# Kernel optimization log

Measured on AMD Instinct MI355X. Metric: run time of the kernel, lower is better.

The kernel has to match this reference:

```python
import jax, jax.numpy as jnp
import numpy as np

N_NODES = 20000
N_EDGES = 200000
N_TOK = 8          # N patch tokens per node
IN_DIM = 64        # C
N_HEADS = 4
HEAD_DIM = 16      # out_dim


def setup_inputs() -> dict:
    key = jax.random.key(0)
    ks = jax.random.split(key, 16)
    scale = 1.0 / np.sqrt(IN_DIM).astype(np.float32)
    def lin(i):
        W = jax.random.normal(ks[i], (IN_DIM, N_HEADS * HEAD_DIM), dtype=jnp.float32) * scale
        b = jax.random.normal(ks[i + 1], (N_HEADS * HEAD_DIM,), dtype=jnp.float32) * 0.01
        return W, b
    Qw, Qb = lin(0)
    Kw, Kb = lin(2)
    Vw, Vb = lin(4)
    Ew, Eb = lin(6)
    h = jax.random.normal(ks[8], (N_NODES, N_TOK, IN_DIM), dtype=jnp.float32)
    e = jax.random.normal(ks[9], (N_EDGES, N_TOK, IN_DIM), dtype=jnp.float32)
    src = jax.random.randint(ks[10], (N_EDGES,), 0, N_NODES)
    dst = jax.random.randint(ks[11], (N_EDGES,), 0, N_NODES)
    return {"h": h, "e": e, "src": src, "dst": dst,
            "Qw": Qw, "Qb": Qb, "Kw": Kw, "Kb": Kb,
            "Vw": Vw, "Vb": Vb, "Ew": Ew, "Eb": Eb}


def _proj(x, W, b):
    # x: [M, N, C] -> [M, N, H, D]
    y = x @ W + b
    return y.reshape(x.shape[0], x.shape[1], N_HEADS, HEAD_DIM)


def reference(h, e, src, dst, Qw, Qb, Kw, Kb, Vw, Vb, Ew, Eb):
    Qh = _proj(h, Qw, Qb)   # [n, N, H, D]
    Kh = _proj(h, Kw, Kb)
    Vh = _proj(h, Vw, Vb)
    pe = _proj(e, Ew, Eb)   # [E, N, H, D]
    inv_sqrt_d = jnp.float32(1.0 / np.sqrt(HEAD_DIM))
    # edge-wise elementwise QK score, scaled, plus relative PE
    score = Kh[src] * Qh[dst] * inv_sqrt_d + pe   # [E, N, H, D]
    e_out = score
    # exp of head-dim-summed clamped score
    s = jnp.exp(jnp.clip(jnp.sum(score, axis=-1, keepdims=True), -5.0, 5.0))  # [E, N, H, 1]
    wV = jax.ops.segment_sum(Vh[src] * s, dst, num_segments=N_NODES)  # [n, N, H, D]
    z = jax.ops.segment_sum(s, dst, num_segments=N_NODES)             # [n, N, H, 1]
    h_out = wV / (z + 1e-6)
    return h_out, e_out
```

## Files before the change

### kernel.cpp

```cpp
#include <hip/hip_runtime.h>
#include <hip/hip_bf16.h>

#define IN_DIM 64
#define N_TOK 8
#define OUT_DIM 64
#define HEAD_DIM 16
#define N_HEADS 4

__global__ void zero_kernel(int* p, int n) {
    int i = blockIdx.x * blockDim.x + threadIdx.x;
    if (i < n) p[i] = 0;
}

__global__ void hist_kernel(const int* __restrict__ dst, int* __restrict__ deg, int n) {
    int i = blockIdx.x * blockDim.x + threadIdx.x;
    if (i < n) atomicAdd(&deg[dst[i]], 1);
}

__global__ void scan_kernel(const int* __restrict__ deg, int* __restrict__ offs,
                            int* __restrict__ cur, int n) {
    __shared__ int buf[1024];
    __shared__ int carry;
    const int tid = threadIdx.x;
    if (tid == 0) carry = 0;
    __syncthreads();
    for (int base = 0; base < n; base += 1024) {
        int i = base + tid;
        int v = (i < n) ? deg[i] : 0;
        buf[tid] = v;
        __syncthreads();
        for (int off = 1; off < 1024; off <<= 1) {
            int t = (tid >= off) ? buf[tid - off] : 0;
            __syncthreads();
            buf[tid] += t;
            __syncthreads();
        }
        int incl = buf[tid];
        int excl = incl - v + carry;
        if (i < n) { offs[i] = excl; cur[i] = excl; }
        __syncthreads();
        if (tid == 0) carry += buf[1023];
        __syncthreads();
    }
    if (tid == 0) offs[n] = carry;
}

__global__ void scatter_kernel(const int* __restrict__ dst, int* __restrict__ cur,
                               int* __restrict__ csr, int n) {
    int i = blockIdx.x * blockDim.x + threadIdx.x;
    if (i < n) {
        int pos = atomicAdd(&cur[dst[i]], 1);
        csr[pos] = i;
    }
}

__device__ __forceinline__ void proj16_acc(const float* __restrict__ tile, int lane,
                                           const float* __restrict__ wb,
                                           float acc[16]) {
#pragma unroll 8
    for (int k = 0; k < 64; ++k) {
        const float ev = tile[lane * 65 + k];
        const float4 w0 = *reinterpret_cast<const float4*>(wb + k * 64);
        const float4 w1 = *reinterpret_cast<const float4*>(wb + k * 64 + 4);
        const float4 w2 = *reinterpret_cast<const float4*>(wb + k * 64 + 8);
        const float4 w3 = *reinterpret_cast<const float4*>(wb + k * 64 + 12);
        acc[0]  = fmaf(ev, w0.x, acc[0]);
        acc[1]  = fmaf(ev, w0.y, acc[1]);
        acc[2]  = fmaf(ev, w0.z, acc[2]);
        acc[3]  = fmaf(ev, w0.w, acc[3]);
        acc[4]  = fmaf(ev, w1.x, acc[4]);
        acc[5]  = fmaf(ev, w1.y, acc[5]);
        acc[6]  = fmaf(ev, w1.z, acc[6]);
        acc[7]  = fmaf(ev, w1.w, acc[7]);
        acc[8]  = fmaf(ev, w2.x, acc[8]);
        acc[9]  = fmaf(ev, w2.y, acc[9]);
        acc[10] = fmaf(ev, w2.z, acc[10]);
        acc[11] = fmaf(ev, w2.w, acc[11]);
        acc[12] = fmaf(ev, w3.x, acc[12]);
        acc[13] = fmaf(ev, w3.y, acc[13]);
        acc[14] = fmaf(ev, w3.z, acc[14]);
        acc[15] = fmaf(ev, w3.w, acc[15]);
    }
}

__device__ __forceinline__ void init16_bias(const float* __restrict__ bb, float acc[16]) {
    const float4 b0 = *reinterpret_cast<const float4*>(bb);
    const float4 b1 = *reinterpret_cast<const float4*>(bb + 4);
    const float4 b2 = *reinterpret_cast<const float4*>(bb + 8);
    const float4 b3 = *reinterpret_cast<const float4*>(bb + 12);
    acc[0] = b0.x;  acc[1] = b0.y;  acc[2] = b0.z;  acc[3] = b0.w;
    acc[4] = b1.x;  acc[5] = b1.y;  acc[6] = b1.z;  acc[7] = b1.w;
    acc[8] = b2.x;  acc[9] = b2.y;  acc[10] = b2.z; acc[11] = b2.w;
    acc[12] = b3.x; acc[13] = b3.y; acc[14] = b3.z; acc[15] = b3.w;
}

__device__ __forceinline__ void store16(float* __restrict__ out, const float acc[16],
                                        float scale) {
    *reinterpret_cast<float4*>(out)      = make_float4(acc[0] * scale, acc[1] * scale,
                                                       acc[2] * scale, acc[3] * scale);
    *reinterpret_cast<float4*>(out + 4)  = make_float4(acc[4] * scale, acc[5] * scale,
                                                       acc[6] * scale, acc[7] * scale);
    *reinterpret_cast<float4*>(out + 8)  = make_float4(acc[8] * scale, acc[9] * scale,
                                                       acc[10] * scale, acc[11] * scale);
    *reinterpret_cast<float4*>(out + 12) = make_float4(acc[12] * scale, acc[13] * scale,
                                                       acc[14] * scale, acc[15] * scale);
}

__global__ void __launch_bounds__(256) hproj_kernel(
    const float* __restrict__ h,
    const float* __restrict__ Qw, const float* __restrict__ Qb,
    const float* __restrict__ Kw, const float* __restrict__ Kb,
    const float* __restrict__ Vw, const float* __restrict__ Vb,
    float* __restrict__ Qh, float* __restrict__ Kh, float* __restrict__ Vh,
    int nrows) {
    __shared__ float tile[64 * 65];
    const int t = threadIdx.x;
    const int lane = t & 63;
    const int chunk = __builtin_amdgcn_readfirstlane(t >> 6);
    const int row0 = blockIdx.x * 64;
    if (row0 >= nrows) return;

#pragma unroll
    for (int i = 0; i < 4; ++i) {
        const int f = i * 1024 + t * 4;
        const float4 v = *reinterpret_cast<const float4*>(h + (size_t)row0 * 64 + f);
        const int r = f >> 6, c = f & 63;
        tile[r * 65 + c + 0] = v.x;
        tile[r * 65 + c + 1] = v.y;
        tile[r * 65 + c + 2] = v.z;
        tile[r * 65 + c + 3] = v.w;
    }
    __syncthreads();

    const int row = row0 + lane;
    const size_t obase = (size_t)row * OUT_DIM + chunk * 16;

    {
        float acc[16];
        init16_bias(Qb + chunk * 16, acc);
        proj16_acc(tile, lane, Qw + chunk * 16, acc);
        store16(Qh + obase, acc, 0.25f);
    }
    {
        float acc[16];
        init16_bias(Kb + chunk * 16, acc);
        proj16_acc(tile, lane, Kw + chunk * 16, acc);
        store16(Kh + obase, acc, 1.0f);
    }
    {
        float acc[16];
        init16_bias(Vb + chunk * 16, acc);
        proj16_acc(tile, lane, Vw + chunk * 16, acc);
        store16(Vh + obase, acc, 1.0f);
    }
}

__global__ void __launch_bounds__(256) edge_kernel(
    const float* __restrict__ e,
    const int* __restrict__ src, const int* __restrict__ dst,
    const float* __restrict__ Ew, const float* __restrict__ Eb,
    const float* __restrict__ Qh, const float* __restrict__ Kh,
    float* __restrict__ e_out, float* __restrict__ s_buf,
    int npairs) {
    __shared__ float tile[64 * 65];
    const int t = threadIdx.x;
    const int lane = t & 63;
    const int chunk = __builtin_amdgcn_readfirstlane(t >> 6);
    const int p0 = blockIdx.x * 64;
    if (p0 >= npairs) return;

#pragma unroll
    for (int i = 0; i < 4; ++i) {
        const int f = i * 1024 + t * 4;
        const float4 v = *reinterpret_cast<const float4*>(e + (size_t)p0 * 64 + f);
        const int r = f >> 6, c = f & 63;
        tile[r * 65 + c + 0] = v.x;
        tile[r * 65 + c + 1] = v.y;
        tile[r * 65 + c + 2] = v.z;
        tile[r * 65 + c + 3] = v.w;
    }

    const int p = p0 + lane;
    const int eidx = p >> 3;
    const int tok = p & 7;
    const int si = src[eidx];
    const int di = dst[eidx];
    const float* krow = Kh + ((size_t)si * N_TOK + tok) * OUT_DIM + chunk * 16;
    const float* qrow = Qh + ((size_t)di * N_TOK + tok) * OUT_DIM + chunk * 16;
    const float4 kv0 = *reinterpret_cast<const float4*>(krow);
    const float4 kv1 = *reinterpret_cast<const float4*>(krow + 4);
    const float4 kv2 = *reinterpret_cast<const float4*>(krow + 8);
    const float4 kv3 = *reinterpret_cast<const float4*>(krow + 12);
    const float4 qv0 = *reinterpret_cast<const float4*>(qrow);
    const float4 qv1 = *reinterpret_cast<const float4*>(qrow + 4);
    const float4 qv2 = *reinterpret_cast<const float4*>(qrow + 8);
    const float4 qv3 = *reinterpret_cast<const float4*>(qrow + 12);

    __syncthreads();

    float acc[16];
    init16_bias(Eb + chunk * 16, acc);
    proj16_acc(tile, lane, Ew + chunk * 16, acc);

    acc[0]  = fmaf(kv0.x, qv0.x, acc[0]);
    acc[1]  = fmaf(kv0.y, qv0.y, acc[1]);
    acc[2]  = fmaf(kv0.z, qv0.z, acc[2]);
    acc[3]  = fmaf(kv0.w, qv0.w, acc[3]);
    acc[4]  = fmaf(kv1.x, qv1.x, acc[4]);
    acc[5]  = fmaf(kv1.y, qv1.y, acc[5]);
    acc[6]  = fmaf(kv1.z, qv1.z, acc[6]);
    acc[7]  = fmaf(kv1.w, qv1.w, acc[7]);
    acc[8]  = fmaf(kv2.x, qv2.x, acc[8]);
    acc[9]  = fmaf(kv2.y, qv2.y, acc[9]);
    acc[10] = fmaf(kv2.z, qv2.z, acc[10]);
    acc[11] = fmaf(kv2.w, qv2.w, acc[11]);
    acc[12] = fmaf(kv3.x, qv3.x, acc[12]);
    acc[13] = fmaf(kv3.y, qv3.y, acc[13]);
    acc[14] = fmaf(kv3.z, qv3.z, acc[14]);
    acc[15] = fmaf(kv3.w, qv3.w, acc[15]);

    float* orow = e_out + (size_t)p * OUT_DIM + chunk * 16;
    *reinterpret_cast<float4*>(orow)      = make_float4(acc[0], acc[1], acc[2], acc[3]);
    *reinterpret_cast<float4*>(orow + 4)  = make_float4(acc[4], acc[5], acc[6], acc[7]);
    *reinterpret_cast<float4*>(orow + 8)  = make_float4(acc[8], acc[9], acc[10], acc[11]);
    *reinterpret_cast<float4*>(orow + 12) = make_float4(acc[12], acc[13], acc[14], acc[15]);

    float s01 = (acc[0] + acc[1]) + (acc[2] + acc[3]);
    float s23 = (acc[4] + acc[5]) + (acc[6] + acc[7]);
    float s45 = (acc[8] + acc[9]) + (acc[10] + acc[11]);
    float s67 = (acc[12] + acc[13]) + (acc[14] + acc[15]);
    float ssum = (s01 + s23) + (s45 + s67);
    ssum = fminf(fmaxf(ssum, -5.f), 5.f);
    s_buf[(size_t)p * N_HEADS + chunk] = __expf(ssum);
}

__global__ void __launch_bounds__(256) gather_kernel(
    const float* __restrict__ Vh, const float* __restrict__ s_buf,
    const int* __restrict__ src,
    const int* __restrict__ offs, const int* __restrict__ csr,
    float* __restrict__ h_out, int nunits) {
    const int unit = blockIdx.x * 4 + (threadIdx.x >> 6);
    const int lane = threadIdx.x & 63;
    if (unit >= nunits) return;
    const int node = unit >> 3;
    const int tok = unit & 7;
    const int beg = offs[node];
    const int end = offs[node + 1];
    const int hh = lane >> 4;
    float acc = 0.f;
    float z = 0.f;
    for (int base = beg; base < end; base += 64) {
        const int n = min(64, end - base);
        int eid = 0, sidx = 0;
        if (lane < n) {
            eid = csr[base + lane];
            sidx = src[eid];
        }
        for (int j = 0; j < n; ++j) {
            const int ej = __shfl(eid, j);
            const int sj = __shfl(sidx, j);
            const float sh = s_buf[((size_t)ej * N_TOK + tok) * N_HEADS + hh];
            const float v = Vh[((size_t)sj * N_TOK + tok) * OUT_DIM + lane];
            acc = fmaf(v, sh, acc);
            z += sh;
        }
    }
    h_out[(size_t)unit * OUT_DIM + lane] = acc / (z + 1e-6f);
}

extern "C" void kernel_launch(void* const* d_in, const int* in_sizes, int n_in,
                              void* d_out, int out_size, void* d_ws, size_t ws_size,
                              hipStream_t stream) {
    const float* h  = (const float*)d_in[0];
    const float* e  = (const float*)d_in[1];
    const int* src  = (const int*)d_in[2];
    const int* dst  = (const int*)d_in[3];
    const float* Qw = (const float*)d_in[4];
    const float* Qb = (const float*)d_in[5];
    const float* Kw = (const float*)d_in[6];
    const float* Kb = (const float*)d_in[7];
    const float* Vw = (const float*)d_in[8];
    const float* Vb = (const float*)d_in[9];
    const float* Ew = (const float*)d_in[10];
    const float* Eb = (const float*)d_in[11];

    const int n_nodes = in_sizes[0] / (N_TOK * IN_DIM);
    const int n_edges = in_sizes[2];
    const int nrows   = n_nodes * N_TOK;
    const int npairs  = n_edges * N_TOK;
    const int h_out_elems = n_nodes * N_TOK * OUT_DIM;

    float* h_out = (float*)d_out;
    float* e_out = (float*)d_out + h_out_elems;

    float* Qh    = (float*)d_ws;
    float* Kh    = Qh + (size_t)nrows * OUT_DIM;
    float* Vh    = Kh + (size_t)nrows * OUT_DIM;
    float* s_buf = Vh + (size_t)nrows * OUT_DIM;
    int*   deg   = (int*)(s_buf + (size_t)npairs * N_HEADS);
    int*   offs  = deg + n_nodes;
    int*   cur   = offs + (n_nodes + 1);
    int*   csr   = cur + n_nodes;

    zero_kernel<<<(n_nodes + 255) / 256, 256, 0, stream>>>(deg, n_nodes);
    hist_kernel<<<(n_edges + 255) / 256, 256, 0, stream>>>(dst, deg, n_edges);
    scan_kernel<<<1, 1024, 0, stream>>>(deg, offs, cur, n_nodes);
    scatter_kernel<<<(n_edges + 255) / 256, 256, 0, stream>>>(dst, cur, csr, n_edges);

    hproj_kernel<<<(nrows + 63) / 64, 256, 0, stream>>>(
        h, Qw, Qb, Kw, Kb, Vw, Vb, Qh, Kh, Vh, nrows);

    edge_kernel<<<(npairs + 63) / 64, 256, 0, stream>>>(
        e, src, dst, Ew, Eb, Qh, Kh, e_out, s_buf, npairs);

    gather_kernel<<<(nrows + 3) / 4, 256, 0, stream>>>(
        Vh, s_buf, src, offs, csr, h_out, nrows);
}
```

Measured before the change: 1.117 ms.

## Coalesce projection and edge stores via LDS, shuffle-based scan, head-major scores

Several changes land together. The scan is replaced with a wavefront-shuffle scan. hproj and edge kernels now stage outputs through LDS so global stores are fully coalesced float4 rows instead of strided per-lane 16-float chunks. The edge kernel gathers K/Q rows cooperatively into LDS tiles. s_buf is stored head-major, and the gather loop is unrolled by two to expose more memory parallelism. This costs more LDS (lower occupancy in edge_kernel) and extra barriers.

```diff
diff --git a/kernel.cpp b/kernel.cpp
--- a/kernel.cpp
+++ b/kernel.cpp
@@ -19,27 +19,40 @@
 
 __global__ void scan_kernel(const int* __restrict__ deg, int* __restrict__ offs,
                             int* __restrict__ cur, int n) {
-    __shared__ int buf[1024];
+    __shared__ int wsum[17];
     __shared__ int carry;
     const int tid = threadIdx.x;
+    const int lane = tid & 63;
+    const int wid = tid >> 6;
     if (tid == 0) carry = 0;
     __syncthreads();
     for (int base = 0; base < n; base += 1024) {
-        int i = base + tid;
-        int v = (i < n) ? deg[i] : 0;
-        buf[tid] = v;
+        const int i = base + tid;
+        const int v = (i < n) ? deg[i] : 0;
+        int x = v;
+#pragma unroll
+        for (int d = 1; d < 64; d <<= 1) {
+            int y = __shfl_up(x, d);
+            if (lane >= d) x += y;
+        }
+        if (lane == 63) wsum[wid] = x;
         __syncthreads();
-        for (int off = 1; off < 1024; off <<= 1) {
-            int t = (tid >= off) ? buf[tid - off] : 0;
-            __syncthreads();
-            buf[tid] += t;
-            __syncthreads();
-        }
-        int incl = buf[tid];
-        int excl = incl - v + carry;
+        if (wid == 0 && lane < 16) {
+            const int a = wsum[lane];
+            int s = a;
+#pragma unroll
+            for (int d = 1; d < 16; d <<= 1) {
+                int y = __shfl_up(s, d);
+                if (lane >= d) s += y;
+            }
+            wsum[lane] = s - a;
+            if (lane == 15) wsum[16] = s;
+        }
+        __syncthreads();
+        const int excl = x - v + wsum[wid] + carry;
         if (i < n) { offs[i] = excl; cur[i] = excl; }
         __syncthreads();
-        if (tid == 0) carry += buf[1023];
+        if (tid == 0) carry += wsum[16];
         __syncthreads();
     }
     if (tid == 0) offs[n] = carry;
@@ -94,18 +107,6 @@
     acc[12] = b3.x; acc[13] = b3.y; acc[14] = b3.z; acc[15] = b3.w;
 }
 
-__device__ __forceinline__ void store16(float* __restrict__ out, const float acc[16],
-                                        float scale) {
-    *reinterpret_cast<float4*>(out)      = make_float4(acc[0] * scale, acc[1] * scale,
-                                                       acc[2] * scale, acc[3] * scale);
-    *reinterpret_cast<float4*>(out + 4)  = make_float4(acc[4] * scale, acc[5] * scale,
-                                                       acc[6] * scale, acc[7] * scale);
-    *reinterpret_cast<float4*>(out + 8)  = make_float4(acc[8] * scale, acc[9] * scale,
-                                                       acc[10] * scale, acc[11] * scale);
-    *reinterpret_cast<float4*>(out + 12) = make_float4(acc[12] * scale, acc[13] * scale,
-                                                       acc[14] * scale, acc[15] * scale);
-}
-
 __global__ void __launch_bounds__(256) hproj_kernel(
     const float* __restrict__ h,
     const float* __restrict__ Qw, const float* __restrict__ Qb,
@@ -132,26 +133,49 @@
     }
     __syncthreads();
 
-    const int row = row0 + lane;
-    const size_t obase = (size_t)row * OUT_DIM + chunk * 16;
-
-    {
-        float acc[16];
-        init16_bias(Qb + chunk * 16, acc);
-        proj16_acc(tile, lane, Qw + chunk * 16, acc);
-        store16(Qh + obase, acc, 0.25f);
-    }
-    {
-        float acc[16];
-        init16_bias(Kb + chunk * 16, acc);
-        proj16_acc(tile, lane, Kw + chunk * 16, acc);
-        store16(Kh + obase, acc, 1.0f);
-    }
-    {
-        float acc[16];
-        init16_bias(Vb + chunk * 16, acc);
-        proj16_acc(tile, lane, Vw + chunk * 16, acc);
-        store16(Vh + obase, acc, 1.0f);
+    float aq[16], ak[16], av[16];
+    init16_bias(Qb + chunk * 16, aq);
+    proj16_acc(tile, lane, Qw + chunk * 16, aq);
+    init16_bias(Kb + chunk * 16, ak);
+    proj16_acc(tile, lane, Kw + chunk * 16, ak);
+    init16_bias(Vb + chunk * 16, av);
+    proj16_acc(tile, lane, Vw + chunk * 16, av);
+
+    __syncthreads();
+#pragma unroll
+    for (int j = 0; j < 16; ++j) tile[lane * 65 + chunk * 16 + j] = aq[j] * 0.25f;
+    __syncthreads();
+#pragma unroll
+    for (int i = 0; i < 4; ++i) {
+        const int f = i * 1024 + t * 4;
+        const int r = f >> 6, c = f & 63;
+        *reinterpret_cast<float4*>(Qh + (size_t)row0 * 64 + f) =
+            make_float4(tile[r * 65 + c], tile[r * 65 + c + 1],
+                        tile[r * 65 + c + 2], tile[r * 65 + c + 3]);
+    }
+    __syncthreads();
+#pragma unroll
+    for (int j = 0; j < 16; ++j) tile[lane * 65 + chunk * 16 + j] = ak[j];
+    __syncthreads();
+#pragma unroll
+    for (int i = 0; i < 4; ++i) {
+        const int f = i * 1024 + t * 4;
+        const int r = f >> 6, c = f & 63;
+        *reinterpret_cast<float4*>(Kh + (size_t)row0 * 64 + f) =
+            make_float4(tile[r * 65 + c], tile[r * 65 + c + 1],
+                        tile[r * 65 + c + 2], tile[r * 65 + c + 3]);
+    }
+    __syncthreads();
+#pragma unroll
+    for (int j = 0; j < 16; ++j) tile[lane * 65 + chunk * 16 + j] = av[j];
+    __syncthreads();
+#pragma unroll
+    for (int i = 0; i < 4; ++i) {
+        const int f = i * 1024 + t * 4;
+        const int r = f >> 6, c = f & 63;
+        *reinterpret_cast<float4*>(Vh + (size_t)row0 * 64 + f) =
+            make_float4(tile[r * 65 + c], tile[r * 65 + c + 1],
+                        tile[r * 65 + c + 2], tile[r * 65 + c + 3]);
     }
 }
 
@@ -161,12 +185,15 @@
     const float* __restrict__ Ew, const float* __restrict__ Eb,
     const float* __restrict__ Qh, const float* __restrict__ Kh,
     float* __restrict__ e_out, float* __restrict__ s_buf,
-    int npairs) {
-    __shared__ float tile[64 * 65];
+    int npairs, int n_edges) {
+    __shared__ float et[64 * 65];
+    __shared__ float kt[64 * 68];
+    __shared__ float qt[64 * 68];
     const int t = threadIdx.x;
     const int lane = t & 63;
     const int chunk = __builtin_amdgcn_readfirstlane(t >> 6);
     const int p0 = blockIdx.x * 64;
+    const int e0 = p0 >> 3;
     if (p0 >= npairs) return;
 
 #pragma unroll
@@ -174,71 +201,73 @@
         const int f = i * 1024 + t * 4;
         const float4 v = *reinterpret_cast<const float4*>(e + (size_t)p0 * 64 + f);
         const int r = f >> 6, c = f & 63;
-        tile[r * 65 + c + 0] = v.x;
-        tile[r * 65 + c + 1] = v.y;
-        tile[r * 65 + c + 2] = v.z;
-        tile[r * 65 + c + 3] = v.w;
-    }
-
-    const int p = p0 + lane;
-    const int eidx = p >> 3;
-    const int tok = p & 7;
-    const int si = src[eidx];
-    const int di = dst[eidx];
-    const float* krow = Kh + ((size_t)si * N_TOK + tok) * OUT_DIM + chunk * 16;
-    const float* qrow = Qh + ((size_t)di * N_TOK + tok) * OUT_DIM + chunk * 16;
-    const float4 kv0 = *reinterpret_cast<const float4*>(krow);
-    const float4 kv1 = *reinterpret_cast<const float4*>(krow + 4);
-    const float4 kv2 = *reinterpret_cast<const float4*>(krow + 8);
-    const float4 kv3 = *reinterpret_cast<const float4*>(krow + 12);
-    const float4 qv0 = *reinterpret_cast<const float4*>(qrow);
-    const float4 qv1 = *reinterpret_cast<const float4*>(qrow + 4);
-    const float4 qv2 = *reinterpret_cast<const float4*>(qrow + 8);
-    const float4 qv3 = *reinterpret_cast<const float4*>(qrow + 12);
-
+        et[r * 65 + c + 0] = v.x;
+        et[r * 65 + c + 1] = v.y;
+        et[r * 65 + c + 2] = v.z;
+        et[r * 65 + c + 3] = v.w;
+    }
+
+    float4* kt4 = reinterpret_cast<float4*>(kt);
+    float4* qt4 = reinterpret_cast<float4*>(qt);
+#pragma unroll
+    for (int i = 0; i < 4; ++i) {
+        const int f = i * 1024 + t * 4;
+        int ee = e0 + (f >> 9);
+        if (ee >= n_edges) ee = n_edges - 1;
+        const int o = f & 511;
+        const int se = src[ee];
+        const int de = dst[ee];
+        const float4 kv = *reinterpret_cast<const float4*>(Kh + (size_t)se * 512 + o);
+        const float4 qv = *reinterpret_cast<const float4*>(Qh + (size_t)de * 512 + o);
+        const int r = f >> 6, c4 = (f & 63) >> 2;
+        kt4[r * 17 + c4] = kv;
+        qt4[r * 17 + c4] = qv;
+    }
     __syncthreads();
 
     float acc[16];
     init16_bias(Eb + chunk * 16, acc);
-    proj16_acc(tile, lane, Ew + chunk * 16, acc);
-
-    acc[0]  = fmaf(kv0.x, qv0.x, acc[0]);
-    acc[1]  = fmaf(kv0.y, qv0.y, acc[1]);
-    acc[2]  = fmaf(kv0.z, qv0.z, acc[2]);
-    acc[3]  = fmaf(kv0.w, qv0.w, acc[3]);
-    acc[4]  = fmaf(kv1.x, qv1.x, acc[4]);
-    acc[5]  = fmaf(kv1.y, qv1.y, acc[5]);
-    acc[6]  = fmaf(kv1.z, qv1.z, acc[6]);
-    acc[7]  = fmaf(kv1.w, qv1.w, acc[7]);
-    acc[8]  = fmaf(kv2.x, qv2.x, acc[8]);
-    acc[9]  = fmaf(kv2.y, qv2.y, acc[9]);
-    acc[10] = fmaf(kv2.z, qv2.z, acc[10]);
-    acc[11] = fmaf(kv2.w, qv2.w, acc[11]);
-    acc[12] = fmaf(kv3.x, qv3.x, acc[12]);
-    acc[13] = fmaf(kv3.y, qv3.y, acc[13]);
-    acc[14] = fmaf(kv3.z, qv3.z, acc[14]);
-    acc[15] = fmaf(kv3.w, qv3.w, acc[15]);
-
-    float* orow = e_out + (size_t)p * OUT_DIM + chunk * 16;
-    *reinterpret_cast<float4*>(orow)      = make_float4(acc[0], acc[1], acc[2], acc[3]);
-    *reinterpret_cast<float4*>(orow + 4)  = make_float4(acc[4], acc[5], acc[6], acc[7]);
-    *reinterpret_cast<float4*>(orow + 8)  = make_float4(acc[8], acc[9], acc[10], acc[11]);
-    *reinterpret_cast<float4*>(orow + 12) = make_float4(acc[12], acc[13], acc[14], acc[15]);
-
-    float s01 = (acc[0] + acc[1]) + (acc[2] + acc[3]);
-    float s23 = (acc[4] + acc[5]) + (acc[6] + acc[7]);
-    float s45 = (acc[8] + acc[9]) + (acc[10] + acc[11]);
-    float s67 = (acc[12] + acc[13]) + (acc[14] + acc[15]);
-    float ssum = (s01 + s23) + (s45 + s67);
-    ssum = fminf(fmaxf(ssum, -5.f), 5.f);
-    s_buf[(size_t)p * N_HEADS + chunk] = __expf(ssum);
+    proj16_acc(et, lane, Ew + chunk * 16, acc);
+
+#pragma unroll
+    for (int c4 = 0; c4 < 4; ++c4) {
+        const float4 kv = kt4[lane * 17 + chunk * 4 + c4];
+        const float4 qv = qt4[lane * 17 + chunk * 4 + c4];
+        acc[c4 * 4 + 0] = fmaf(kv.x, qv.x, acc[c4 * 4 + 0]);
+        acc[c4 * 4 + 1] = fmaf(kv.y, qv.y, acc[c4 * 4 + 1]);
+        acc[c4 * 4 + 2] = fmaf(kv.z, qv.z, acc[c4 * 4 + 2]);
+        acc[c4 * 4 + 3] = fmaf(kv.w, qv.w, acc[c4 * 4 + 3]);
+    }
+
+    {
+        float s01 = (acc[0] + acc[1]) + (acc[2] + acc[3]);
+        float s23 = (acc[4] + acc[5]) + (acc[6] + acc[7]);
+        float s45 = (acc[8] + acc[9]) + (acc[10] + acc[11]);
+        float s67 = (acc[12] + acc[13]) + (acc[14] + acc[15]);
+        float ssum = (s01 + s23) + (s45 + s67);
+        ssum = fminf(fmaxf(ssum, -5.f), 5.f);
+        s_buf[(size_t)chunk * npairs + p0 + lane] = __expf(ssum);
+    }
+
+    __syncthreads();
+#pragma unroll
+    for (int j = 0; j < 16; ++j) et[lane * 65 + chunk * 16 + j] = acc[j];
+    __syncthreads();
+#pragma unroll
+    for (int i = 0; i < 4; ++i) {
+        const int f = i * 1024 + t * 4;
+        const int r = f >> 6, c = f & 63;
+        *reinterpret_cast<float4*>(e_out + (size_t)p0 * 64 + f) =
+            make_float4(et[r * 65 + c], et[r * 65 + c + 1],
+                        et[r * 65 + c + 2], et[r * 65 + c + 3]);
+    }
 }
 
 __global__ void __launch_bounds__(256) gather_kernel(
     const float* __restrict__ Vh, const float* __restrict__ s_buf,
     const int* __restrict__ src,
     const int* __restrict__ offs, const int* __restrict__ csr,
-    float* __restrict__ h_out, int nunits) {
+    float* __restrict__ h_out, int nunits, int npairs) {
     const int unit = blockIdx.x * 4 + (threadIdx.x >> 6);
     const int lane = threadIdx.x & 63;
     if (unit >= nunits) return;
@@ -247,22 +276,33 @@
     const int beg = offs[node];
     const int end = offs[node + 1];
     const int hh = lane >> 4;
+    const float* sb = s_buf + (size_t)hh * npairs + tok;
     float acc = 0.f;
     float z = 0.f;
     for (int base = beg; base < end; base += 64) {
-        const int n = min(64, end - base);
+        const int nn = min(64, end - base);
         int eid = 0, sidx = 0;
-        if (lane < n) {
+        if (lane < nn) {
             eid = csr[base + lane];
             sidx = src[eid];
         }
-        for (int j = 0; j < n; ++j) {
+        int j = 0;
+        for (; j + 1 < nn; j += 2) {
+            const int ej0 = __shfl(eid, j),     ej1 = __shfl(eid, j + 1);
+            const int sj0 = __shfl(sidx, j),    sj1 = __shfl(sidx, j + 1);
+            const float sh0 = sb[(size_t)ej0 * 8];
+            const float sh1 = sb[(size_t)ej1 * 8];
+            const float v0 = Vh[((size_t)sj0 * 8 + tok) * 64 + lane];
+            const float v1 = Vh[((size_t)sj1 * 8 + tok) * 64 + lane];
+            acc = fmaf(v0, sh0, acc); z += sh0;
+            acc = fmaf(v1, sh1, acc); z += sh1;
+        }
+        if (j < nn) {
             const int ej = __shfl(eid, j);
             const int sj = __shfl(sidx, j);
-            const float sh = s_buf[((size_t)ej * N_TOK + tok) * N_HEADS + hh];
-            const float v = Vh[((size_t)sj * N_TOK + tok) * OUT_DIM + lane];
-            acc = fmaf(v, sh, acc);
-            z += sh;
+            const float sh = sb[(size_t)ej * 8];
+            const float v = Vh[((size_t)sj * 8 + tok) * 64 + lane];
+            acc = fmaf(v, sh, acc); z += sh;
         }
     }
     h_out[(size_t)unit * OUT_DIM + lane] = acc / (z + 1e-6f);
@@ -311,8 +351,8 @@
         h, Qw, Qb, Kw, Kb, Vw, Vb, Qh, Kh, Vh, nrows);
 
     edge_kernel<<<(npairs + 63) / 64, 256, 0, stream>>>(
-        e, src, dst, Ew, Eb, Qh, Kh, e_out, s_buf, npairs);
+        e, src, dst, Ew, Eb, Qh, Kh, e_out, s_buf, npairs, n_edges);
 
     gather_kernel<<<(nrows + 3) / 4, 256, 0, stream>>>(
-        Vh, s_buf, src, offs, csr, h_out, nrows);
-}
+        Vh, s_buf, src, offs, csr, h_out, nrows, npairs);
+}
```

After: 990.4 us. -11.3%, faster.
